# Optimization experiments

Measured on AMD Instinct MI355X. Metric: run time of the kernel, lower is better.

Reference implementation:

```python
import jax, jax.numpy as jnp
import numpy as np

B, LI, LT = 1, 2048, 256
H, NH, HD, MLP = 1024, 16, 64, 4096
L = LI + LT


def _make_pe():
    pos = jnp.arange(L, dtype=jnp.float32)[:, None]
    omega = 1.0 / (10000.0 ** (jnp.arange(0, HD, 2, dtype=jnp.float32) / HD))  # [HD/2]
    ang = pos * omega[None, :]                                                 # [L, HD/2]
    cos, sin = jnp.cos(ang), jnp.sin(ang)
    rot = jnp.stack([jnp.stack([cos, -sin], -1), jnp.stack([sin, cos], -1)], -2)  # [L, HD/2, 2, 2]
    return rot[None, None].astype(jnp.float32)                                 # [1,1,L,HD/2,2,2]


def setup_inputs() -> dict:
    key = jax.random.key(0)
    ks = jax.random.split(key, 20)
    w = lambda k, s: jax.random.normal(k, s, jnp.float32) * 0.02
    return {
        'img': jax.random.normal(ks[0], (B, LI, H), jnp.float32),
        'txt': jax.random.normal(ks[1], (B, LT, H), jnp.float32),
        'pe': _make_pe(),
        'vec': jax.random.normal(ks[2], (B, H), jnp.float32),
        'img_mod_w': w(ks[3], (H, 6 * H)), 'img_mod_b': w(ks[4], (6 * H,)),
        'txt_mod_w': w(ks[5], (H, 6 * H)), 'txt_mod_b': w(ks[6], (6 * H,)),
        'img_qkv_w': w(ks[7], (H, 3 * H)), 'img_qkv_b': w(ks[8], (3 * H,)),
        'img_q_scale': jnp.ones((HD,), jnp.float32), 'img_k_scale': jnp.ones((HD,), jnp.float32),
        'img_proj_w': w(ks[9], (H, H)), 'img_proj_b': w(ks[10], (H,)),
        'txt_qkv_w': w(ks[11], (H, 3 * H)), 'txt_qkv_b': w(ks[12], (3 * H,)),
        'txt_q_scale': jnp.ones((HD,), jnp.float32), 'txt_k_scale': jnp.ones((HD,), jnp.float32),
        'mlp_w1': w(ks[13], (H, MLP)), 'mlp_b1': w(ks[14], (MLP,)),
        'mlp_w2': w(ks[15], (MLP, H)), 'mlp_b2': w(ks[16], (H,)),
    }


def _ln(x):  # LayerNorm, no affine, eps=1e-6
    m = jnp.mean(x, -1, keepdims=True)
    v = jnp.mean((x - m) ** 2, -1, keepdims=True)
    return (x - m) * jax.lax.rsqrt(v + 1e-6)


def _rms(x, scale):  # QKNorm RMSNorm, eps=1e-6, learned per-dim scale
    return x * jax.lax.rsqrt(jnp.mean(x * x, -1, keepdims=True) + 1e-6) * scale


def _qkv_heads(x, w, b):
    b_, l_, _ = x.shape
    qkv = (jnp.einsum('bld,de->ble', x, w) + b).reshape(b_, l_, 3, NH, HD)
    qkv = jnp.transpose(qkv, (2, 0, 3, 1, 4))  # [3,B,H,L,D]
    return qkv[0], qkv[1], qkv[2]


def _rope(x, pe):
    xr = x.reshape(x.shape[:-1] + (HD // 2, 1, 2))  # [B,H,L,HD/2,1,2]
    out = pe[..., 0] * xr[..., 0] + pe[..., 1] * xr[..., 1]
    return out.reshape(x.shape)


def reference(img, txt, pe, vec, img_mod_w, img_mod_b, txt_mod_w, txt_mod_b,
              img_qkv_w, img_qkv_b, img_q_scale, img_k_scale, img_proj_w, img_proj_b,
              txt_qkv_w, txt_qkv_b, txt_q_scale, txt_k_scale,
              mlp_w1, mlp_b1, mlp_w2, mlp_b2):
    sv = jax.nn.silu(vec)
    imod = (jnp.einsum('bd,de->be', sv, img_mod_w) + img_mod_b)[:, None, :]
    i_shift1, i_scale1, i_gate1, i_shift2, i_scale2, i_gate2 = jnp.split(imod, 6, -1)
    tmod = (jnp.einsum('bd,de->be', sv, txt_mod_w) + txt_mod_b)[:, None, :]
    t_shift1, t_scale1 = jnp.split(tmod, 6, -1)[0], jnp.split(tmod, 6, -1)[1]

    img_m = (1 + i_scale1) * _ln(img) + i_shift1
    iq, ik, iv = _qkv_heads(img_m, img_qkv_w, img_qkv_b)
    iq, ik = _rms(iq, img_q_scale), _rms(ik, img_k_scale)

    txt_m = (1 + t_scale1) * _ln(txt) + t_shift1
    tq, tk, tv = _qkv_heads(txt_m, txt_qkv_w, txt_qkv_b)
    tq, tk = _rms(tq, txt_q_scale), _rms(tk, txt_k_scale)

    q = _rope(jnp.concatenate([tq, iq], 2), pe)
    k = _rope(jnp.concatenate([tk, ik], 2), pe)
    v = jnp.concatenate([tv, iv], 2)

    scores = jnp.einsum('bhqd,bhkd->bhqk', q, k) / np.float32(np.sqrt(HD))
    attn = jnp.einsum('bhqk,bhkd->bhqd', jax.nn.softmax(scores, -1), v)
    attn = jnp.transpose(attn, (0, 2, 1, 3)).reshape(attn.shape[0], L, NH * HD)

    img_attn = attn[:, txt.shape[1]:]
    img = img + i_gate1 * (jnp.einsum('bld,de->ble', img_attn, img_proj_w) + img_proj_b)
    h = (1 + i_scale2) * _ln(img) + i_shift2
    h = jax.nn.gelu(jnp.einsum('bld,de->ble', h, mlp_w1) + mlp_b1, approximate=True)
    h = jnp.einsum('bld,de->ble', h, mlp_w2) + mlp_b2
    return img + i_gate2 * h
```

## Files before the change

kernel.cpp:

```cpp
#include <hip/hip_runtime.h>
#include <cstdint>
#include <cstddef>

typedef unsigned short u16;
typedef __attribute__((ext_vector_type(8))) short bf16x8;
typedef __attribute__((ext_vector_type(4))) float f32x4;

#define AS1 __attribute__((address_space(1)))
#define AS3 __attribute__((address_space(3)))
#define GLDS16(g, s) __builtin_amdgcn_global_load_lds((const AS1 void*)(g), (AS3 void*)(s), 16, 0, 0)

__device__ inline u16 f2bf(float f) {
  union { float f; unsigned u; } c; c.f = f;
  unsigned r = c.u + 0x7fffu + ((c.u >> 16) & 1u);
  return (u16)(r >> 16);
}
__device__ inline float bf2f(u16 s) {
  union { unsigned u; float f; } c; c.u = ((unsigned)s) << 16;
  return c.f;
}
__device__ inline unsigned cvt_pk_bf16(float a, float b) {
  unsigned r;
  asm("v_cvt_pk_bf16_f32 %0, %1, %2" : "=v"(r) : "v"(a), "v"(b));
  return r;
}

__global__ __launch_bounds__(256)
void wconv_t(const float* __restrict__ W, u16* __restrict__ Wt, int K, int N) {
  __shared__ float tile[32][33];
  const int tx = threadIdx.x, ty = threadIdx.y;
  const int n0 = blockIdx.x * 32, k0 = blockIdx.y * 32;
#pragma unroll
  for (int i = 0; i < 4; ++i)
    tile[ty + i * 8][tx] = W[(size_t)(k0 + ty + i * 8) * N + n0 + tx];
  __syncthreads();
#pragma unroll
  for (int i = 0; i < 4; ++i)
    Wt[(size_t)(n0 + ty + i * 8) * K + k0 + tx] = f2bf(tile[tx][ty + i * 8]);
}

__global__ __launch_bounds__(256)
void silu_kernel(const float* __restrict__ vec, float* __restrict__ sv) {
  int i = blockIdx.x * 256 + threadIdx.x;
  float x = vec[i];
  sv[i] = x / (1.f + __expf(-x));
}

__global__ __launch_bounds__(256)
void modinit(const float* __restrict__ imb, const float* __restrict__ tmb, float* __restrict__ mod) {
  int i = blockIdx.x * 256 + threadIdx.x;
  mod[i] = (i < 6144) ? imb[i] : tmb[i - 6144];
}

__global__ __launch_bounds__(256)
void modgemv(const float* __restrict__ sv, const float* __restrict__ imw,
             const float* __restrict__ tmw, float* __restrict__ mod) {
  __shared__ float s[128];
  const int t = threadIdx.x;
  const int c = blockIdx.x * 256 + t;
  const int kc = blockIdx.y * 128;
  if (t < 128) s[t] = sv[kc + t];
  __syncthreads();
  const float* W; int col;
  if (c < 6144) { W = imw; col = c; } else { W = tmw; col = c - 6144; }
  float acc = 0.f;
#pragma unroll 8
  for (int k = 0; k < 128; ++k) acc += s[k] * W[(size_t)(kc + k) * 6144 + col];
  atomicAdd(&mod[c], acc);
}

__global__ __launch_bounds__(256)
void ln_mod(const float* __restrict__ x, const float* __restrict__ shift,
            const float* __restrict__ scale, u16* __restrict__ out) {
  const int row = blockIdx.x, t = threadIdx.x;
  const float* xr = x + (size_t)row * 1024;
  float v[4], s = 0.f, sq = 0.f;
#pragma unroll
  for (int i = 0; i < 4; ++i) { v[i] = xr[t + i * 256]; s += v[i]; sq += v[i] * v[i]; }
#pragma unroll
  for (int o = 32; o; o >>= 1) { s += __shfl_down(s, o); sq += __shfl_down(sq, o); }
  __shared__ float ls[8];
  if ((t & 63) == 0) { ls[t >> 6] = s; ls[4 + (t >> 6)] = sq; }
  __syncthreads();
  s = ls[0] + ls[1] + ls[2] + ls[3];
  sq = ls[4] + ls[5] + ls[6] + ls[7];
  const float mean = s * (1.f / 1024.f);
  const float var = sq * (1.f / 1024.f) - mean * mean;
  const float rstd = rsqrtf(var + 1e-6f);
#pragma unroll
  for (int i = 0; i < 4; ++i) {
    int c = t + i * 256;
    float xn = (v[i] - mean) * rstd;
    out[(size_t)row * 1024 + c] = f2bf((1.f + scale[c]) * xn + shift[c]);
  }
}

template <int EPI, int BM, int BN>
__global__ __launch_bounds__(256, 3)
void gemm_bt(const u16* __restrict__ A, const u16* __restrict__ Bt,
             int M, int N, int Kstride, int Kspan,
             const float* __restrict__ bias, const float* __restrict__ gate,
             const float* __restrict__ resid, void* __restrict__ Cout) {
  constexpr int MF = BM / 32, NF = BN / 32, L = (BM + BN) / 64;
  __shared__ u16 smA[2][BM * 32];
  __shared__ u16 smB[2][BN * 32];
  const int t = threadIdx.x;
  const int w = t >> 6, l = t & 63;
  const int lr = l & 15, lg = l >> 4;
  const int m0 = blockIdx.x * BM, n0 = blockIdx.y * BN;
  const int koff = blockIdx.z * Kspan;
  const int wm = (w >> 1) * (BM / 2), wn = (w & 1) * (BN / 2);
  f32x4 acc[MF][NF] = {};

  const u16* gb[L];
  int doff[L];
  bool isA[L];
#pragma unroll
  for (int i = 0; i < L; ++i) {
    int c = t + i * 256;
    if (c < BM * 4) {
      int row = c >> 2, ch = c & 3;
      gb[i] = A + (size_t)(m0 + row) * Kstride + koff + ((ch ^ ((row >> 1) & 3)) << 3);
      doff[i] = c * 8; isA[i] = true;
    } else {
      int cc = c - BM * 4, row = cc >> 2, ch = cc & 3;
      gb[i] = Bt + (size_t)(n0 + row) * Kstride + koff + ((ch ^ ((row >> 1) & 3)) << 3);
      doff[i] = cc * 8; isA[i] = false;
    }
  }
  auto stage = [&](int kt, int b) {
#pragma unroll
    for (int i = 0; i < L; ++i)
      GLDS16(gb[i] + (kt << 5), (isA[i] ? smA[b] : smB[b]) + doff[i]);
  };

  const int nk = Kspan >> 5;
  stage(0, 0);
  for (int kt = 0; kt < nk; ++kt) {
    const int b = kt & 1;
    if (kt < nk - 1) {
      stage(kt + 1, b ^ 1);
      if constexpr (L == 4)      asm volatile("s_waitcnt vmcnt(4)" ::: "memory");
      else if constexpr (L == 3) asm volatile("s_waitcnt vmcnt(3)" ::: "memory");
      else                       asm volatile("s_waitcnt vmcnt(2)" ::: "memory");
    } else {
      asm volatile("s_waitcnt vmcnt(0)" ::: "memory");
    }
    __builtin_amdgcn_s_barrier();
    asm volatile("" ::: "memory");

    bf16x8 af[MF], bfr[NF];
#pragma unroll
    for (int m = 0; m < MF; ++m) {
      int row = wm + m * 16 + lr;
      af[m] = *(const bf16x8*)(smA[b] + row * 32 + ((lg ^ ((row >> 1) & 3)) << 3));
    }
#pragma unroll
    for (int n = 0; n < NF; ++n) {
      int row = wn + n * 16 + lr;
      bfr[n] = *(const bf16x8*)(smB[b] + row * 32 + ((lg ^ ((row >> 1) & 3)) << 3));
    }
    __builtin_amdgcn_s_setprio(1);
#pragma unroll
    for (int m = 0; m < MF; ++m)
#pragma unroll
      for (int n = 0; n < NF; ++n)
        acc[m][n] = __builtin_amdgcn_mfma_f32_16x16x32_bf16(af[m], bfr[n], acc[m][n], 0, 0, 0);
    __builtin_amdgcn_s_setprio(0);
    asm volatile("" ::: "memory");
    __builtin_amdgcn_s_barrier();
  }

#pragma unroll
  for (int m = 0; m < MF; ++m) {
    const int row = m0 + wm + m * 16 + lg * 4;
#pragma unroll
    for (int n = 0; n < NF; ++n) {
      const int col = n0 + wn + n * 16 + lr;
#pragma unroll
      for (int i = 0; i < 4; ++i) {
        float v = acc[m][n][i];
        size_t idx = (size_t)(row + i) * N + col;
        if constexpr (EPI == 0) {
          ((u16*)Cout)[idx] = f2bf(v + bias[col]);
        } else if constexpr (EPI == 2) {
          float cc = v + bias[col];
          float u = 0.7978845608f * (cc + 0.044715f * cc * cc * cc);
          float e = __expf(2.f * u);
          float th = 1.f - 2.f / (e + 1.f);
          ((u16*)Cout)[idx] = f2bf(0.5f * cc * (1.f + th));
        } else if constexpr (EPI == 4) {
          ((float*)Cout)[(size_t)blockIdx.z * M * N + idx] = v;
        } else {
          ((float*)Cout)[idx] = resid[idx] + gate[col] * (v + bias[col]);
        }
      }
    }
  }
}

__global__ __launch_bounds__(256)
void combine2(const float* __restrict__ part, const float* __restrict__ bias,
              const float* __restrict__ gate, const float* __restrict__ resid,
              float* __restrict__ out) {
  size_t idx = (size_t)blockIdx.x * 256 + threadIdx.x;
  int col = (int)(idx & 1023);
  float v = part[idx] + part[(size_t)2048 * 1024 + idx] + bias[col];
  out[idx] = resid[idx] + gate[col] * v;
}

__global__ __launch_bounds__(256)
void qk_post(const u16* __restrict__ qkv_txt, const u16* __restrict__ qkv_img,
             const float* __restrict__ pe,
             const float* __restrict__ iq_s, const float* __restrict__ ik_s,
             const float* __restrict__ tq_s, const float* __restrict__ tk_s,
             u16* __restrict__ Q, u16* __restrict__ K) {
  const int d = threadIdx.x;
  const int pos = blockIdx.x * 4 + threadIdx.y;
  const int h = blockIdx.y;
  const u16* src; int r; const float *qs, *ks;
  if (pos < 256) { src = qkv_txt; r = pos; qs = tq_s; ks = tk_s; }
  else           { src = qkv_img; r = pos - 256; qs = iq_s; ks = ik_s; }
  float q = bf2f(src[(size_t)r * 3072 + h * 64 + d]);
  float k = bf2f(src[(size_t)r * 3072 + 1024 + h * 64 + d]);
  float qsq = q * q, ksq = k * k;
#pragma unroll
  for (int o = 32; o; o >>= 1) { qsq += __shfl_xor(qsq, o); ksq += __shfl_xor(ksq, o); }
  q *= rsqrtf(qsq * (1.f / 64.f) + 1e-6f) * qs[d];
  k *= rsqrtf(ksq * (1.f / 64.f) + 1e-6f) * ks[d];
  const int p = d >> 1, odd = d & 1;
  const float* pp = pe + (((size_t)pos * 32 + p) * 2 + odd) * 2;
  float qp = __shfl_xor(q, 1), kp = __shfl_xor(k, 1);
  float qe = odd ? qp : q, qo = odd ? q : qp;
  float ke = odd ? kp : k, ko = odd ? k : kp;
  float rq = pp[0] * qe + pp[1] * qo;
  float rk = pp[0] * ke + pp[1] * ko;
  size_t oidx = ((size_t)h * 2304 + pos) * 64 + d;
  Q[oidx] = f2bf(rq * 0.125f);
  K[oidx] = f2bf(rk);
}

__global__ __launch_bounds__(512)
void v_transpose(const u16* __restrict__ qkv_txt, const u16* __restrict__ qkv_img,
                 u16* __restrict__ Vt) {
  __shared__ float tile[64][65];
  const int tx = threadIdx.x, ty = threadIdx.y;
  const int p0 = blockIdx.x * 64, h = blockIdx.y;
#pragma unroll
  for (int i = 0; i < 8; ++i) {
    int pos = p0 + ty + i * 8;
    const u16* src; int r;
    if (pos < 256) { src = qkv_txt; r = pos; } else { src = qkv_img; r = pos - 256; }
    tile[ty + i * 8][tx] = bf2f(src[(size_t)r * 3072 + 2048 + h * 64 + tx]);
  }
  __syncthreads();
#pragma unroll
  for (int i = 0; i < 8; ++i) {
    int d = ty + i * 8;
    Vt[((size_t)h * 64 + d) * 2304 + p0 + tx] = f2bf(tile[tx][d]);
  }
}

__global__ __launch_bounds__(256, 3)
void attn_kernel(const u16* __restrict__ Q, const u16* __restrict__ Kb,
                 const u16* __restrict__ Vt,
                 float* __restrict__ Opart, float* __restrict__ ml) {
  __shared__ u16 smK[2][64 * 64];
  __shared__ u16 smV[2][64 * 64];
  __shared__ u16 smP[4 * 16 * 72];
  const int t = threadIdx.x, w = t >> 6, l = t & 63;
  const int lr = l & 15, lg = l >> 4;
  const int qt = blockIdx.x, h = blockIdx.y, sp = blockIdx.z;
  const int j0 = sp * 18;
  const u16* Qp = Q + ((size_t)h * 2304 + qt * 64 + w * 16 + lr) * 64;
  const bf16x8 qf0 = *(const bf16x8*)(Qp + lg * 8);
  const bf16x8 qf1 = *(const bf16x8*)(Qp + 32 + lg * 8);
  const u16* Kbase = Kb + (size_t)h * 2304 * 64;
  const u16* Vbase = Vt + (size_t)h * 64 * 2304;
  f32x4 accO[4] = {};
  float mrun = -1e30f, lrun = 0.f;
  u16* myP = smP + w * (16 * 72);

  const int c0 = w * 64 + l, c1 = c0 + 256;
  const int kr0 = c0 >> 3, ks0 = ((c0 & 7) ^ (kr0 & 7)) * 8;
  const int kr1 = c1 >> 3, ks1 = ((c1 & 7) ^ (kr1 & 7)) * 8;

  auto stage = [&](int j, int b) {
    const u16* gK = Kbase + (size_t)j * 64 * 64;
    GLDS16(gK + (size_t)kr0 * 64 + ks0, smK[b] + (w * 64) * 8);
    GLDS16(gK + (size_t)kr1 * 64 + ks1, smK[b] + (256 + w * 64) * 8);
    GLDS16(Vbase + (size_t)kr0 * 2304 + j * 64 + ks0, smV[b] + (w * 64) * 8);
    GLDS16(Vbase + (size_t)kr1 * 2304 + j * 64 + ks1, smV[b] + (256 + w * 64) * 8);
  };

  stage(j0, 0);
  for (int jj = 0; jj < 18; ++jj) {
    const int b = jj & 1;
    if (jj < 17) {
      stage(j0 + jj + 1, b ^ 1);
      asm volatile("s_waitcnt vmcnt(4)" ::: "memory");
    } else {
      asm volatile("s_waitcnt vmcnt(0)" ::: "memory");
    }
    __builtin_amdgcn_s_barrier();
    asm volatile("" ::: "memory");

    f32x4 sf[4];
    __builtin_amdgcn_s_setprio(1);
#pragma unroll
    for (int n = 0; n < 4; ++n) {
      const int row = n * 16 + lr, sw = row & 7;
      bf16x8 kf0 = *(const bf16x8*)(smK[b] + row * 64 + ((lg ^ sw) << 3));
      bf16x8 kf1 = *(const bf16x8*)(smK[b] + row * 64 + (((lg + 4) ^ sw) << 3));
      f32x4 z = {};
      z = __builtin_amdgcn_mfma_f32_16x16x32_bf16(kf0, qf0, z, 0, 0, 0);
      z = __builtin_amdgcn_mfma_f32_16x16x32_bf16(kf1, qf1, z, 0, 0, 0);
      sf[n] = z;
    }
    __builtin_amdgcn_s_setprio(0);

    float t0 = fmaxf(fmaxf(sf[0][0], sf[0][1]), fmaxf(sf[0][2], sf[0][3]));
    float t1 = fmaxf(fmaxf(sf[1][0], sf[1][1]), fmaxf(sf[1][2], sf[1][3]));
    float t2 = fmaxf(fmaxf(sf[2][0], sf[2][1]), fmaxf(sf[2][2], sf[2][3]));
    float t3 = fmaxf(fmaxf(sf[3][0], sf[3][1]), fmaxf(sf[3][2], sf[3][3]));
    float mx = fmaxf(fmaxf(t0, t1), fmaxf(t2, t3));
    mx = fmaxf(mx, __shfl_xor(mx, 16));
    mx = fmaxf(mx, __shfl_xor(mx, 32));
    const float mnew = fmaxf(mrun, mx);
    const float corr = __expf(mrun - mnew);
    mrun = mnew;

    float p[4][4];
#pragma unroll
    for (int n = 0; n < 4; ++n) {
      p[n][0] = __expf(sf[n][0] - mnew);
      p[n][1] = __expf(sf[n][1] - mnew);
      p[n][2] = __expf(sf[n][2] - mnew);
      p[n][3] = __expf(sf[n][3] - mnew);
    }
    float s0 = (p[0][0] + p[0][1]) + (p[0][2] + p[0][3]);
    float s1 = (p[1][0] + p[1][1]) + (p[1][2] + p[1][3]);
    float s2 = (p[2][0] + p[2][1]) + (p[2][2] + p[2][3]);
    float s3 = (p[3][0] + p[3][1]) + (p[3][2] + p[3][3]);
    float rs = (s0 + s1) + (s2 + s3);
    rs += __shfl_xor(rs, 16);
    rs += __shfl_xor(rs, 32);
    lrun = lrun * corr + rs;

#pragma unroll
    for (int n = 0; n < 4; ++n) {
      *(unsigned*)(myP + lr * 72 + n * 16 + lg * 4)     = cvt_pk_bf16(p[n][0], p[n][1]);
      *(unsigned*)(myP + lr * 72 + n * 16 + lg * 4 + 2) = cvt_pk_bf16(p[n][2], p[n][3]);
    }

    float cb[4];
#pragma unroll
    for (int i = 0; i < 4; ++i) cb[i] = __shfl(corr, lg * 4 + i);
#pragma unroll
    for (int nd = 0; nd < 4; ++nd)
#pragma unroll
      for (int i = 0; i < 4; ++i) accO[nd][i] *= cb[i];

    __builtin_amdgcn_s_setprio(1);
#pragma unroll
    for (int c = 0; c < 2; ++c) {
      bf16x8 pf = *(const bf16x8*)(myP + lr * 72 + c * 32 + lg * 8);
#pragma unroll
      for (int nd = 0; nd < 4; ++nd) {
        const int row = nd * 16 + lr, sw = row & 7;
        bf16x8 vf = *(const bf16x8*)(smV[b] + row * 64 + (((c * 4 + lg) ^ sw) << 3));
        accO[nd] = __builtin_amdgcn_mfma_f32_16x16x32_bf16(pf, vf, accO[nd], 0, 0, 0);
      }
    }
    __builtin_amdgcn_s_setprio(0);
    asm volatile("" ::: "memory");
    __builtin_amdgcn_s_barrier();
  }

  float* Op = Opart + (((size_t)(sp * 16 + h) * 2304) + qt * 64) * 64;
#pragma unroll
  for (int nd = 0; nd < 4; ++nd)
#pragma unroll
    for (int i = 0; i < 4; ++i)
      Op[(size_t)(w * 16 + lg * 4 + i) * 64 + nd * 16 + lr] = accO[nd][i];
  if (lg == 0) {
    size_t mi = ((size_t)(sp * 16 + h) * 2304 + qt * 64 + w * 16 + lr) * 2;
    ml[mi] = mrun;
    ml[mi + 1] = lrun;
  }
}

__global__ __launch_bounds__(256)
void attn_combine(const float* __restrict__ Opart, const float* __restrict__ ml,
                  u16* __restrict__ outb) {
  int idx = blockIdx.x * 256 + threadIdx.x;
  int q = idx >> 10, c = idx & 1023;
  int h = c >> 6, d = c & 63;
  size_t i0 = (size_t)h * 2304 + q;
  size_t i1 = (size_t)(16 + h) * 2304 + q;
  float m0 = ml[i0 * 2], l0 = ml[i0 * 2 + 1];
  float m1 = ml[i1 * 2], l1 = ml[i1 * 2 + 1];
  float M = fmaxf(m0, m1);
  float w0 = __expf(m0 - M), w1 = __expf(m1 - M);
  float a0 = Opart[i0 * 64 + d], a1 = Opart[i1 * 64 + d];
  float num = w0 * a0 + w1 * a1;
  float den = w0 * l0 + w1 * l1;
  outb[(size_t)q * 1024 + c] = f2bf(num / den);
}

extern "C" void kernel_launch(void* const* d_in, const int* in_sizes, int n_in,
                              void* d_out, int out_size, void* d_ws, size_t ws_size,
                              hipStream_t stream) {
  const float* img         = (const float*)d_in[0];
  const float* txt         = (const float*)d_in[1];
  const float* pe          = (const float*)d_in[2];
  const float* vec         = (const float*)d_in[3];
  const float* img_mod_w   = (const float*)d_in[4];
  const float* img_mod_b   = (const float*)d_in[5];
  const float* txt_mod_w   = (const float*)d_in[6];
  const float* txt_mod_b   = (const float*)d_in[7];
  const float* img_qkv_w   = (const float*)d_in[8];
  const float* img_qkv_b   = (const float*)d_in[9];
  const float* img_q_scale = (const float*)d_in[10];
  const float* img_k_scale = (const float*)d_in[11];
  const float* img_proj_w  = (const float*)d_in[12];
  const float* img_proj_b  = (const float*)d_in[13];
  const float* txt_qkv_w   = (const float*)d_in[14];
  const float* txt_qkv_b   = (const float*)d_in[15];
  const float* txt_q_scale = (const float*)d_in[16];
  const float* txt_k_scale = (const float*)d_in[17];
  const float* mlp_w1      = (const float*)d_in[18];
  const float* mlp_b1      = (const float*)d_in[19];
  const float* mlp_w2      = (const float*)d_in[20];
  const float* mlp_b2      = (const float*)d_in[21];
  (void)in_sizes; (void)n_in; (void)out_size; (void)ws_size;

  char* ws = (char*)d_ws;
  size_t off = 0;
  auto alloc = [&](size_t bytes) -> void* {
    void* p = ws + off;
    off += (bytes + 255) & ~(size_t)255;
    return p;
  };
  float* sv     = (float*)alloc(1024 * 4);
  float* mod    = (float*)alloc(8192 * 4);
  u16* qkv_img  = (u16*)alloc((size_t)2048 * 3072 * 2);
  u16* qkv_txt  = (u16*)alloc((size_t)256 * 3072 * 2);
  u16* img_m    = (u16*)alloc((size_t)2048 * 1024 * 2);
  u16* txt_m    = (u16*)alloc((size_t)256 * 1024 * 2);
  float* Opart  = (float*)qkv_img;
  float* pml2   = (float*)qkv_img;
  float* mlbuf  = (float*)alloc((size_t)2 * 16 * 2304 * 2 * 4);
  u16* wt_iqkv  = (u16*)alloc((size_t)3072 * 1024 * 2);
  u16* wt_tqkv  = (u16*)alloc((size_t)3072 * 1024 * 2);
  u16* wt_proj  = (u16*)alloc((size_t)1024 * 1024 * 2);
  u16* wt_m1    = (u16*)alloc((size_t)4096 * 1024 * 2);
  u16* wt_m2    = (u16*)alloc((size_t)1024 * 4096 * 2);
  u16* Qb       = (u16*)alloc((size_t)16 * 2304 * 64 * 2);
  u16* Kb       = (u16*)alloc((size_t)16 * 2304 * 64 * 2);
  u16* Vtb      = (u16*)alloc((size_t)16 * 64 * 2304 * 2);
  u16* attnb    = (u16*)alloc((size_t)2304 * 1024 * 2);
  float* img2   = (float*)alloc((size_t)2048 * 1024 * 4);
  u16* h_in     = (u16*)alloc((size_t)2048 * 1024 * 2);
  u16* h1       = (u16*)alloc((size_t)2048 * 4096 * 2);

  const dim3 bT(32, 8);
  wconv_t<<<dim3(3072 / 32, 1024 / 32), bT, 0, stream>>>(img_qkv_w, wt_iqkv, 1024, 3072);
  wconv_t<<<dim3(3072 / 32, 1024 / 32), bT, 0, stream>>>(txt_qkv_w, wt_tqkv, 1024, 3072);
  wconv_t<<<dim3(1024 / 32, 1024 / 32), bT, 0, stream>>>(img_proj_w, wt_proj, 1024, 1024);
  wconv_t<<<dim3(4096 / 32, 1024 / 32), bT, 0, stream>>>(mlp_w1, wt_m1, 1024, 4096);
  wconv_t<<<dim3(1024 / 32, 4096 / 32), bT, 0, stream>>>(mlp_w2, wt_m2, 4096, 1024);

  silu_kernel<<<4, 256, 0, stream>>>(vec, sv);
  modinit<<<32, 256, 0, stream>>>(img_mod_b, txt_mod_b, mod);
  modgemv<<<dim3(32, 8), 256, 0, stream>>>(sv, img_mod_w, txt_mod_w, mod);

  ln_mod<<<2048, 256, 0, stream>>>(img, mod + 0, mod + 1024, img_m);
  ln_mod<<<256, 256, 0, stream>>>(txt, mod + 6144, mod + 7168, txt_m);

  gemm_bt<0, 128, 128><<<dim3(16, 24), 256, 0, stream>>>(img_m, wt_iqkv, 2048, 3072, 1024, 1024,
                                                         img_qkv_b, nullptr, nullptr, qkv_img);
  gemm_bt<0, 128, 128><<<dim3(2, 24), 256, 0, stream>>>(txt_m, wt_tqkv, 256, 3072, 1024, 1024,
                                                        txt_qkv_b, nullptr, nullptr, qkv_txt);

  qk_post<<<dim3(576, 16), dim3(64, 4), 0, stream>>>(qkv_txt, qkv_img, pe,
                                                     img_q_scale, img_k_scale,
                                                     txt_q_scale, txt_k_scale, Qb, Kb);
  v_transpose<<<dim3(36, 16), dim3(64, 8), 0, stream>>>(qkv_txt, qkv_img, Vtb);

  attn_kernel<<<dim3(36, 16, 2), 256, 0, stream>>>(Qb, Kb, Vtb, Opart, mlbuf);
  attn_combine<<<9216, 256, 0, stream>>>(Opart, mlbuf, attnb);

  gemm_bt<1, 64, 64><<<dim3(32, 16), 256, 0, stream>>>(attnb + (size_t)256 * 1024, wt_proj,
                                                       2048, 1024, 1024, 1024,
                                                       img_proj_b, mod + 2048, img, img2);
  ln_mod<<<2048, 256, 0, stream>>>(img2, mod + 3072, mod + 4096, h_in);
  gemm_bt<2, 128, 128><<<dim3(16, 32), 256, 0, stream>>>(h_in, wt_m1, 2048, 4096, 1024, 1024,
                                                         mlp_b1, nullptr, nullptr, h1);
  gemm_bt<4, 64, 64><<<dim3(32, 16, 2), 256, 0, stream>>>(h1, wt_m2, 2048, 1024, 4096, 2048,
                                                          nullptr, nullptr, nullptr, pml2);
  combine2<<<8192, 256, 0, stream>>>(pml2, mlp_b2, mod + 5120, img2, (float*)d_out);
}
```

Measured before the change: 411.9 us.

## Merge conversion and layernorm launches, use exp2 softmax, retile GEMMs, swizzle P tile

Folds the five weight transpose/convert launches into one kernel, and the image and text LayerNorm-modulate launches into one. Attention now pre-multiplies Q by log2(e)/sqrt(d) and uses exp2f, including in the split combine, so each exponential needs one less multiply. The P tile in shared memory moves from a padded layout to an XOR-swizzled one, and attention launch bounds rise to 4 blocks. The QKV and MLP1 GEMMs switch to 64x128 tiles for more blocks, which trades lower per-block data reuse for better occupancy and load balance.

```diff
diff --git a/kernel.cpp b/kernel.cpp
--- a/kernel.cpp
+++ b/kernel.cpp
@@ -26,10 +26,22 @@
 }
 
 __global__ __launch_bounds__(256)
-void wconv_t(const float* __restrict__ W, u16* __restrict__ Wt, int K, int N) {
+void wconv_all(const float* __restrict__ w_iqkv, const float* __restrict__ w_tqkv,
+               const float* __restrict__ w_proj, const float* __restrict__ w_m1,
+               const float* __restrict__ w_m2,
+               u16* __restrict__ o_iqkv, u16* __restrict__ o_tqkv,
+               u16* __restrict__ o_proj, u16* __restrict__ o_m1, u16* __restrict__ o_m2) {
   __shared__ float tile[32][33];
   const int tx = threadIdx.x, ty = threadIdx.y;
-  const int n0 = blockIdx.x * 32, k0 = blockIdx.y * 32;
+  int bid = blockIdx.x;
+  const float* W; u16* Wt; int K, N, local;
+  if (bid < 3072)       { W = w_iqkv; Wt = o_iqkv; K = 1024; N = 3072; local = bid; }
+  else if (bid < 6144)  { W = w_tqkv; Wt = o_tqkv; K = 1024; N = 3072; local = bid - 3072; }
+  else if (bid < 7168)  { W = w_proj; Wt = o_proj; K = 1024; N = 1024; local = bid - 6144; }
+  else if (bid < 11264) { W = w_m1;   Wt = o_m1;   K = 1024; N = 4096; local = bid - 7168; }
+  else                  { W = w_m2;   Wt = o_m2;   K = 4096; N = 1024; local = bid - 11264; }
+  const int nb = N >> 5;
+  const int n0 = (local % nb) * 32, k0 = (local / nb) * 32;
 #pragma unroll
   for (int i = 0; i < 4; ++i)
     tile[ty + i * 8][tx] = W[(size_t)(k0 + ty + i * 8) * N + n0 + tx];
@@ -70,10 +82,12 @@
 }
 
 __global__ __launch_bounds__(256)
-void ln_mod(const float* __restrict__ x, const float* __restrict__ shift,
-            const float* __restrict__ scale, u16* __restrict__ out) {
+void ln_mod2(const float* __restrict__ ximg, const float* __restrict__ xtxt,
+             const float* __restrict__ mod, u16* __restrict__ oimg, u16* __restrict__ otxt) {
   const int row = blockIdx.x, t = threadIdx.x;
-  const float* xr = x + (size_t)row * 1024;
+  const float* xr; const float *shift, *scale; u16* out; int r;
+  if (row < 2048) { r = row; xr = ximg + (size_t)r * 1024; shift = mod;        scale = mod + 1024; out = oimg; }
+  else            { r = row - 2048; xr = xtxt + (size_t)r * 1024; shift = mod + 6144; scale = mod + 7168; out = otxt; }
   float v[4], s = 0.f, sq = 0.f;
 #pragma unroll
   for (int i = 0; i < 4; ++i) { v[i] = xr[t + i * 256]; s += v[i]; sq += v[i] * v[i]; }
@@ -91,7 +105,7 @@
   for (int i = 0; i < 4; ++i) {
     int c = t + i * 256;
     float xn = (v[i] - mean) * rstd;
-    out[(size_t)row * 1024 + c] = f2bf((1.f + scale[c]) * xn + shift[c]);
+    out[(size_t)r * 1024 + c] = f2bf((1.f + scale[c]) * xn + shift[c]);
   }
 }
 
@@ -236,7 +250,7 @@
   float rq = pp[0] * qe + pp[1] * qo;
   float rk = pp[0] * ke + pp[1] * ko;
   size_t oidx = ((size_t)h * 2304 + pos) * 64 + d;
-  Q[oidx] = f2bf(rq * 0.125f);
+  Q[oidx] = f2bf(rq * 0.1803368801111204f);
   K[oidx] = f2bf(rk);
 }
 
@@ -261,13 +275,13 @@
   }
 }
 
-__global__ __launch_bounds__(256, 3)
+__global__ __launch_bounds__(256, 4)
 void attn_kernel(const u16* __restrict__ Q, const u16* __restrict__ Kb,
                  const u16* __restrict__ Vt,
                  float* __restrict__ Opart, float* __restrict__ ml) {
   __shared__ u16 smK[2][64 * 64];
   __shared__ u16 smV[2][64 * 64];
-  __shared__ u16 smP[4 * 16 * 72];
+  __shared__ u16 smP[4][16 * 64];
   const int t = threadIdx.x, w = t >> 6, l = t & 63;
   const int lr = l & 15, lg = l >> 4;
   const int qt = blockIdx.x, h = blockIdx.y, sp = blockIdx.z;
@@ -279,7 +293,7 @@
   const u16* Vbase = Vt + (size_t)h * 64 * 2304;
   f32x4 accO[4] = {};
   float mrun = -1e30f, lrun = 0.f;
-  u16* myP = smP + w * (16 * 72);
+  u16* myP = smP[w];
 
   const int c0 = w * 64 + l, c1 = c0 + 256;
   const int kr0 = c0 >> 3, ks0 = ((c0 & 7) ^ (kr0 & 7)) * 8;
@@ -327,16 +341,16 @@
     mx = fmaxf(mx, __shfl_xor(mx, 16));
     mx = fmaxf(mx, __shfl_xor(mx, 32));
     const float mnew = fmaxf(mrun, mx);
-    const float corr = __expf(mrun - mnew);
+    const float corr = exp2f(mrun - mnew);
     mrun = mnew;
 
     float p[4][4];
 #pragma unroll
     for (int n = 0; n < 4; ++n) {
-      p[n][0] = __expf(sf[n][0] - mnew);
-      p[n][1] = __expf(sf[n][1] - mnew);
-      p[n][2] = __expf(sf[n][2] - mnew);
-      p[n][3] = __expf(sf[n][3] - mnew);
+      p[n][0] = exp2f(sf[n][0] - mnew);
+      p[n][1] = exp2f(sf[n][1] - mnew);
+      p[n][2] = exp2f(sf[n][2] - mnew);
+      p[n][3] = exp2f(sf[n][3] - mnew);
     }
     float s0 = (p[0][0] + p[0][1]) + (p[0][2] + p[0][3]);
     float s1 = (p[1][0] + p[1][1]) + (p[1][2] + p[1][3]);
@@ -349,8 +363,10 @@
 
 #pragma unroll
     for (int n = 0; n < 4; ++n) {
-      *(unsigned*)(myP + lr * 72 + n * 16 + lg * 4)     = cvt_pk_bf16(p[n][0], p[n][1]);
-      *(unsigned*)(myP + lr * 72 + n * 16 + lg * 4 + 2) = cvt_pk_bf16(p[n][2], p[n][3]);
+      const int cA = (2 * n + (lg >> 1)) ^ (lr & 7);
+      u16* base = myP + lr * 64 + cA * 8 + (lg & 1) * 4;
+      *(unsigned*)(base)     = cvt_pk_bf16(p[n][0], p[n][1]);
+      *(unsigned*)(base + 2) = cvt_pk_bf16(p[n][2], p[n][3]);
     }
 
     float cb[4];
@@ -364,7 +380,7 @@
     __builtin_amdgcn_s_setprio(1);
 #pragma unroll
     for (int c = 0; c < 2; ++c) {
-      bf16x8 pf = *(const bf16x8*)(myP + lr * 72 + c * 32 + lg * 8);
+      bf16x8 pf = *(const bf16x8*)(myP + lr * 64 + (((4 * c + lg) ^ (lr & 7)) << 3));
 #pragma unroll
       for (int nd = 0; nd < 4; ++nd) {
         const int row = nd * 16 + lr, sw = row & 7;
@@ -401,7 +417,7 @@
   float m0 = ml[i0 * 2], l0 = ml[i0 * 2 + 1];
   float m1 = ml[i1 * 2], l1 = ml[i1 * 2 + 1];
   float M = fmaxf(m0, m1);
-  float w0 = __expf(m0 - M), w1 = __expf(m1 - M);
+  float w0 = exp2f(m0 - M), w1 = exp2f(m1 - M);
   float a0 = Opart[i0 * 64 + d], a1 = Opart[i1 * 64 + d];
   float num = w0 * a0 + w1 * a1;
   float den = w0 * l0 + w1 * l1;
@@ -464,24 +480,19 @@
   u16* h_in     = (u16*)alloc((size_t)2048 * 1024 * 2);
   u16* h1       = (u16*)alloc((size_t)2048 * 4096 * 2);
 
-  const dim3 bT(32, 8);
-  wconv_t<<<dim3(3072 / 32, 1024 / 32), bT, 0, stream>>>(img_qkv_w, wt_iqkv, 1024, 3072);
-  wconv_t<<<dim3(3072 / 32, 1024 / 32), bT, 0, stream>>>(txt_qkv_w, wt_tqkv, 1024, 3072);
-  wconv_t<<<dim3(1024 / 32, 1024 / 32), bT, 0, stream>>>(img_proj_w, wt_proj, 1024, 1024);
-  wconv_t<<<dim3(4096 / 32, 1024 / 32), bT, 0, stream>>>(mlp_w1, wt_m1, 1024, 4096);
-  wconv_t<<<dim3(1024 / 32, 4096 / 32), bT, 0, stream>>>(mlp_w2, wt_m2, 4096, 1024);
+  wconv_all<<<15360, dim3(32, 8), 0, stream>>>(img_qkv_w, txt_qkv_w, img_proj_w, mlp_w1, mlp_w2,
+                                               wt_iqkv, wt_tqkv, wt_proj, wt_m1, wt_m2);
 
   silu_kernel<<<4, 256, 0, stream>>>(vec, sv);
   modinit<<<32, 256, 0, stream>>>(img_mod_b, txt_mod_b, mod);
   modgemv<<<dim3(32, 8), 256, 0, stream>>>(sv, img_mod_w, txt_mod_w, mod);
 
-  ln_mod<<<2048, 256, 0, stream>>>(img, mod + 0, mod + 1024, img_m);
-  ln_mod<<<256, 256, 0, stream>>>(txt, mod + 6144, mod + 7168, txt_m);
-
-  gemm_bt<0, 128, 128><<<dim3(16, 24), 256, 0, stream>>>(img_m, wt_iqkv, 2048, 3072, 1024, 1024,
-                                                         img_qkv_b, nullptr, nullptr, qkv_img);
-  gemm_bt<0, 128, 128><<<dim3(2, 24), 256, 0, stream>>>(txt_m, wt_tqkv, 256, 3072, 1024, 1024,
-                                                        txt_qkv_b, nullptr, nullptr, qkv_txt);
+  ln_mod2<<<2304, 256, 0, stream>>>(img, txt, mod, img_m, txt_m);
+
+  gemm_bt<0, 64, 128><<<dim3(32, 24), 256, 0, stream>>>(img_m, wt_iqkv, 2048, 3072, 1024, 1024,
+                                                        img_qkv_b, nullptr, nullptr, qkv_img);
+  gemm_bt<0, 64, 128><<<dim3(4, 24), 256, 0, stream>>>(txt_m, wt_tqkv, 256, 3072, 1024, 1024,
+                                                       txt_qkv_b, nullptr, nullptr, qkv_txt);
 
   qk_post<<<dim3(576, 16), dim3(64, 4), 0, stream>>>(qkv_txt, qkv_img, pe,
                                                      img_q_scale, img_k_scale,
@@ -494,9 +505,9 @@
   gemm_bt<1, 64, 64><<<dim3(32, 16), 256, 0, stream>>>(attnb + (size_t)256 * 1024, wt_proj,
                                                        2048, 1024, 1024, 1024,
                                                        img_proj_b, mod + 2048, img, img2);
-  ln_mod<<<2048, 256, 0, stream>>>(img2, mod + 3072, mod + 4096, h_in);
-  gemm_bt<2, 128, 128><<<dim3(16, 32), 256, 0, stream>>>(h_in, wt_m1, 2048, 4096, 1024, 1024,
-                                                         mlp_b1, nullptr, nullptr, h1);
+  ln_mod2<<<2048, 256, 0, stream>>>(img2, nullptr, mod + 3072, h_in, nullptr);
+  gemm_bt<2, 64, 128><<<dim3(32, 32), 256, 0, stream>>>(h_in, wt_m1, 2048, 4096, 1024, 1024,
+                                                        mlp_b1, nullptr, nullptr, h1);
   gemm_bt<4, 64, 64><<<dim3(32, 16, 2), 256, 0, stream>>>(h1, wt_m2, 2048, 1024, 4096, 2048,
                                                           nullptr, nullptr, nullptr, pml2);
   combine2<<<8192, 256, 0, stream>>>(pml2, mlp_b2, mod + 5120, img2, (float*)d_out);
```

Result: no change. 405.8 us (-1.5%).
